# Performance work log

Measured on AMD Instinct MI355X. Metric: run time of the kernel, lower is better.

The kernel has to match this reference:

```python
import jax, jax.numpy as jnp
import numpy as np

TEMPERATURE = 0.5
BATCH_SIZE = 4096
EPS = 1e-8  # torch.nn.CosineSimilarity default eps


def setup_inputs() -> dict:
    key = jax.random.key(0)
    k1, k2 = jax.random.split(key)
    z1 = jax.random.normal(k1, (BATCH_SIZE, 256), dtype=jnp.float32)
    z2 = jax.random.normal(k2, (BATCH_SIZE, 256), dtype=jnp.float32)
    return {"z1": z1, "z2": z2}


def reference(z1, z2):
    B = z1.shape[0]
    N = 2 * B
    reps = jnp.concatenate([z1, z2], axis=0)  # [N, D]
    # Cosine similarity (torch clamps each norm to eps before dividing)
    norms = jnp.maximum(jnp.linalg.norm(reps, axis=1, keepdims=True), EPS)
    z = reps / norms
    sim = z @ z.T  # [N, N] cosine similarity matrix

    # positives: diagonals at offsets +B and -B (they are identical by symmetry,
    # but keep the original concat order: [diag(+B), diag(-B)])
    l_pos = jnp.diagonal(sim, offset=B)
    r_pos = jnp.diagonal(sim, offset=-B)
    positives = jnp.concatenate([l_pos, r_pos])  # [N]

    inv_t = 1.0 / TEMPERATURE
    pos_logit = positives * inv_t  # logits[:, 0]

    # negatives are all off-diagonal entries of each row (the positive pair is
    # thus present twice in the logits, faithful to the original). CE with
    # label 0 => loss_i = logsumexp(logits_i) - logits_i[0].
    neg_logits = jnp.where(jnp.eye(N, dtype=bool), -jnp.inf, sim * inv_t)
    lse = jnp.logaddexp(pos_logit, jax.scipy.special.logsumexp(neg_logits, axis=1))
    loss = jnp.sum(lse - pos_logit) / N
    return loss
```

## Files before the change

### kernel.cpp

```cpp
#include <hip/hip_runtime.h>
#include <hip/hip_bf16.h>
#include <cstdint>
#include <cstddef>
#include <math.h>

#define BSZ   4096
#define NROW  8192
#define DIM   256
#define INV_T 2.0f
#define EPS_N 1e-8f

typedef __attribute__((ext_vector_type(4))) float f32x4;

__device__ __forceinline__ void load_lds16(const void* g, void* l) {
    __builtin_amdgcn_global_load_lds(
        (const __attribute__((address_space(1))) void*)g,
        (__attribute__((address_space(3))) void*)l,
        16, 0, 0);
}

__global__ __launch_bounds__(256)
void nt_normalize(const float* __restrict__ z1,
                  const float* __restrict__ z2,
                  char* __restrict__ zn3,
                  float* __restrict__ rowsum) {
    const int wave = threadIdx.x >> 6;
    const int lane = threadIdx.x & 63;
    const int row  = blockIdx.x * 4 + wave;
    const float* src = (row < BSZ) ? (z1 + (size_t)row * DIM)
                                   : (z2 + (size_t)(row - BSZ) * DIM);
    const float4 v = ((const float4*)src)[lane];
    float ss = v.x * v.x + v.y * v.y + v.z * v.z + v.w * v.w;
    #pragma unroll
    for (int off = 32; off; off >>= 1) ss += __shfl_xor(ss, off);
    const float rinv = 1.0f / fmaxf(sqrtf(ss), EPS_N);
    int pk = 0;
    pk = __builtin_amdgcn_cvt_pk_fp8_f32(v.x * rinv, v.y * rinv, pk, false);
    pk = __builtin_amdgcn_cvt_pk_fp8_f32(v.z * rinv, v.w * rinv, pk, true);
    const int s    = row >> 7;
    const int lrow = row & 127;
    const int kc   = lane >> 4;
    const int unit = (lane >> 1) & 7;
    const int off4 = (lane & 1) * 4;
    const int u    = unit ^ (lrow & 7);
    *(int*)(zn3 + (size_t)s * 32768 + kc * 8192 + lrow * 64 + u * 8 + off4) = pk;
    if (lane == 0) rowsum[row] = 0.0f;
}

__global__ __launch_bounds__(256)
void nt_gram(const char* __restrict__ zn3,
             float* __restrict__ rowsum,
             float* __restrict__ pos) {
    const int l = blockIdx.x;
    int bi = (int)((129.0 - sqrt(16641.0 - 8.0 * (double)l)) * 0.5);
    while (64 * (bi + 1) - (bi + 1) * bi / 2 <= l) ++bi;
    while (64 * bi - bi * (bi - 1) / 2 > l) --bi;
    const int bj = bi + (l - (64 * bi - bi * (bi - 1) / 2));

    __shared__ char As[8192];
    __shared__ char Bs[8192];

    const int t    = threadIdx.x;
    const int lane = t & 63;
    const int wave = t >> 6;
    const int wrow = (wave >> 1) * 64;
    const int wcol = (wave & 1) * 64;
    const int q    = lane >> 4;
    const int r16  = lane & 15;
    const int sw   = r16 & 7;
    const int t16  = t * 16;

    const char* A2 = zn3 + (size_t)bi * 32768;
    const char* B2 = zn3 + (size_t)bj * 32768;

    f32x4 acc[4][4] = {};

    for (int kc = 0; kc < 4; ++kc) {
        load_lds16(A2 + kc * 8192 + t16,        As + t16);
        load_lds16(A2 + kc * 8192 + 4096 + t16, As + 4096 + t16);
        load_lds16(B2 + kc * 8192 + t16,        Bs + t16);
        load_lds16(B2 + kc * 8192 + 4096 + t16, Bs + 4096 + t16);
        __syncthreads();

        #pragma unroll
        for (int kh = 0; kh < 2; ++kh) {
            const int spos = (((kh << 2) + q) ^ sw) << 3;
            long af[4], bfv[4];
            #pragma unroll
            for (int mi = 0; mi < 4; ++mi)
                af[mi] = *(const long*)(As + (wrow + mi * 16 + r16) * 64 + spos);
            #pragma unroll
            for (int ni = 0; ni < 4; ++ni)
                bfv[ni] = *(const long*)(Bs + (wcol + ni * 16 + r16) * 64 + spos);
            #pragma unroll
            for (int mi = 0; mi < 4; ++mi)
                #pragma unroll
                for (int ni = 0; ni < 4; ++ni)
                    acc[mi][ni] = __builtin_amdgcn_mfma_f32_16x16x32_fp8_fp8(
                        af[mi], bfv[ni], acc[mi][ni], 0, 0, 0);
        }
        __syncthreads();
    }

    const int c = r16;
    const bool diag_block = (bi == bj);
    float colp[4] = {0.f, 0.f, 0.f, 0.f};

    #pragma unroll
    for (int mi = 0; mi < 4; ++mi) {
        #pragma unroll
        for (int r = 0; r < 4; ++r) {
            const int grow = bi * 128 + wrow + mi * 16 + q * 4 + r;
            float s = 0.f;
            #pragma unroll
            for (int ni = 0; ni < 4; ++ni) {
                const int gcol = bj * 128 + wcol + ni * 16 + c;
                const float val = acc[mi][ni][r];
                float e = __expf(val * INV_T);
                e = (grow == gcol) ? 0.f : e;
                s += e;
                colp[ni] += e;
                if (gcol == grow + BSZ) {
                    pos[grow] = val;
                    pos[gcol] = val;
                }
            }
            s += __shfl_xor(s, 1);
            s += __shfl_xor(s, 2);
            s += __shfl_xor(s, 4);
            s += __shfl_xor(s, 8);
            if (c == 0) atomicAdd(&rowsum[grow], s);
        }
    }
    if (!diag_block) {
        #pragma unroll
        for (int ni = 0; ni < 4; ++ni) {
            float cs = colp[ni];
            cs += __shfl_xor(cs, 16);
            cs += __shfl_xor(cs, 32);
            if (q == 0) atomicAdd(&rowsum[bj * 128 + wcol + ni * 16 + c], cs);
        }
    }
}

__global__ __launch_bounds__(1024)
void nt_finalize(const float* __restrict__ rowsum,
                 const float* __restrict__ pos,
                 float* __restrict__ out) {
    const float4* rs4 = (const float4*)rowsum;
    const float4* ps4 = (const float4*)pos;
    float v = 0.f;
    #pragma unroll
    for (int it = 0; it < 2; ++it) {
        const int i = it * 1024 + threadIdx.x;
        const float4 r = rs4[i];
        const float4 p = ps4[i];
        v += logf(__expf(p.x * INV_T) + r.x) - p.x * INV_T;
        v += logf(__expf(p.y * INV_T) + r.y) - p.y * INV_T;
        v += logf(__expf(p.z * INV_T) + r.z) - p.z * INV_T;
        v += logf(__expf(p.w * INV_T) + r.w) - p.w * INV_T;
    }
    #pragma unroll
    for (int off = 32; off; off >>= 1) v += __shfl_xor(v, off);
    __shared__ float redf[16];
    if ((threadIdx.x & 63) == 0) redf[threadIdx.x >> 6] = v;
    __syncthreads();
    if (threadIdx.x == 0) {
        float s = 0.f;
        #pragma unroll
        for (int w = 0; w < 16; ++w) s += redf[w];
        out[0] = s * (1.0f / NROW);
    }
}

extern "C" void kernel_launch(void* const* d_in, const int* in_sizes, int n_in,
                              void* d_out, int out_size, void* d_ws, size_t ws_size,
                              hipStream_t stream) {
    const float* z1 = (const float*)d_in[0];
    const float* z2 = (const float*)d_in[1];
    float* out = (float*)d_out;

    char*  zn3    = (char*)d_ws;
    float* rowsum = (float*)((char*)d_ws + (size_t)NROW * DIM);
    float* pos    = rowsum + NROW;

    nt_normalize<<<NROW / 4, 256, 0, stream>>>(z1, z2, zn3, rowsum);
    nt_gram<<<2080, 256, 0, stream>>>(zn3, rowsum, pos);
    nt_finalize<<<1, 1024, 0, stream>>>(rowsum, pos, out);
}
```

Baseline: 100.8 us.

## Replace rowsum atomics with per-slot partial buffer and parallel finalize

After: 94.79 us. 1.06x faster.

```diff
diff --git a/kernel.cpp b/kernel.cpp
--- a/kernel.cpp
+++ b/kernel.cpp
@@ -23,7 +23,7 @@
 void nt_normalize(const float* __restrict__ z1,
                   const float* __restrict__ z2,
                   char* __restrict__ zn3,
-                  float* __restrict__ rowsum) {
+                  unsigned int* __restrict__ cnt) {
     const int wave = threadIdx.x >> 6;
     const int lane = threadIdx.x & 63;
     const int row  = blockIdx.x * 4 + wave;
@@ -44,12 +44,12 @@
     const int off4 = (lane & 1) * 4;
     const int u    = unit ^ (lrow & 7);
     *(int*)(zn3 + (size_t)s * 32768 + kc * 8192 + lrow * 64 + u * 8 + off4) = pk;
-    if (lane == 0) rowsum[row] = 0.0f;
+    if (row == 0 && lane == 0) *cnt = 0;
 }
 
 __global__ __launch_bounds__(256)
 void nt_gram(const char* __restrict__ zn3,
-             float* __restrict__ rowsum,
+             float* __restrict__ part,
              float* __restrict__ pos) {
     const int l = blockIdx.x;
     int bi = (int)((129.0 - sqrt(16641.0 - 8.0 * (double)l)) * 0.5);
@@ -104,6 +104,8 @@
 
     const int c = r16;
     const bool diag_block = (bi == bj);
+    const int rslot = 2 * bj + (wcol >> 6);
+    const int cslot = 2 * bi + (wrow >> 6);
     float colp[4] = {0.f, 0.f, 0.f, 0.f};
 
     #pragma unroll
@@ -129,7 +131,7 @@
             s += __shfl_xor(s, 2);
             s += __shfl_xor(s, 4);
             s += __shfl_xor(s, 8);
-            if (c == 0) atomicAdd(&rowsum[grow], s);
+            if (c == 0) part[(size_t)grow * 128 + rslot] = s;
         }
     }
     if (!diag_block) {
@@ -138,38 +140,54 @@
             float cs = colp[ni];
             cs += __shfl_xor(cs, 16);
             cs += __shfl_xor(cs, 32);
-            if (q == 0) atomicAdd(&rowsum[bj * 128 + wcol + ni * 16 + c], cs);
+            if (q == 0)
+                part[(size_t)(bj * 128 + wcol + ni * 16 + c) * 128 + cslot] = cs;
         }
     }
 }
 
-__global__ __launch_bounds__(1024)
-void nt_finalize(const float* __restrict__ rowsum,
+__global__ __launch_bounds__(256)
+void nt_finalize(const float* __restrict__ part,
                  const float* __restrict__ pos,
+                 float* __restrict__ blocksum,
+                 unsigned int* __restrict__ cnt,
                  float* __restrict__ out) {
-    const float4* rs4 = (const float4*)rowsum;
-    const float4* ps4 = (const float4*)pos;
-    float v = 0.f;
-    #pragma unroll
-    for (int it = 0; it < 2; ++it) {
-        const int i = it * 1024 + threadIdx.x;
-        const float4 r = rs4[i];
-        const float4 p = ps4[i];
-        v += logf(__expf(p.x * INV_T) + r.x) - p.x * INV_T;
-        v += logf(__expf(p.y * INV_T) + r.y) - p.y * INV_T;
-        v += logf(__expf(p.z * INV_T) + r.z) - p.z * INV_T;
-        v += logf(__expf(p.w * INV_T) + r.w) - p.w * INV_T;
-    }
-    #pragma unroll
-    for (int off = 32; off; off >>= 1) v += __shfl_xor(v, off);
-    __shared__ float redf[16];
-    if ((threadIdx.x & 63) == 0) redf[threadIdx.x >> 6] = v;
+    const int b    = blockIdx.x;
+    const int t    = threadIdx.x;
+    const int lane = t & 63;
+    const int row  = b * 128 + (t >> 1);
+    const int half = t & 1;
+
+    const float4* p4 = (const float4*)(part + (size_t)row * 128 + half * 64);
+    float s = 0.f;
+    #pragma unroll
+    for (int j = 0; j < 16; ++j) {
+        const float4 v = p4[j];
+        s += v.x + v.y + v.z + v.w;
+    }
+    s += __shfl_xor(s, 1);
+    float contrib = 0.f;
+    if (half == 0) {
+        const float pl = pos[row] * INV_T;
+        contrib = logf(__expf(pl) + s) - pl;
+    }
+    #pragma unroll
+    for (int off = 32; off; off >>= 1) contrib += __shfl_xor(contrib, off);
+    __shared__ float r4[4];
+    __shared__ int   slast;
+    if (lane == 0) r4[t >> 6] = contrib;
     __syncthreads();
-    if (threadIdx.x == 0) {
-        float s = 0.f;
-        #pragma unroll
-        for (int w = 0; w < 16; ++w) s += redf[w];
-        out[0] = s * (1.0f / NROW);
+    if (t == 0) {
+        blocksum[b] = r4[0] + r4[1] + r4[2] + r4[3];
+        __threadfence();
+        slast = (atomicAdd(cnt, 1u) == 63u);
+    }
+    __syncthreads();
+    if (slast && t < 64) {
+        float v = atomicAdd(&blocksum[t], 0.0f);
+        #pragma unroll
+        for (int off = 32; off; off >>= 1) v += __shfl_xor(v, off);
+        if (t == 0) out[0] = v * (1.0f / NROW);
     }
 }
 
@@ -180,11 +198,13 @@
     const float* z2 = (const float*)d_in[1];
     float* out = (float*)d_out;
 
-    char*  zn3    = (char*)d_ws;
-    float* rowsum = (float*)((char*)d_ws + (size_t)NROW * DIM);
-    float* pos    = rowsum + NROW;
-
-    nt_normalize<<<NROW / 4, 256, 0, stream>>>(z1, z2, zn3, rowsum);
-    nt_gram<<<2080, 256, 0, stream>>>(zn3, rowsum, pos);
-    nt_finalize<<<1, 1024, 0, stream>>>(rowsum, pos, out);
-}
+    char*  zn3      = (char*)d_ws;
+    float* part     = (float*)((char*)d_ws + (size_t)2097152);
+    float* pos      = (float*)((char*)d_ws + (size_t)6291456);
+    float* blocksum = pos + NROW;
+    unsigned int* cnt = (unsigned int*)(blocksum + 64);
+
+    nt_normalize<<<NROW / 4, 256, 0, stream>>>(z1, z2, zn3, cnt);
+    nt_gram<<<2080, 256, 0, stream>>>(zn3, part, pos);
+    nt_finalize<<<64, 256, 0, stream>>>(part, pos, blocksum, cnt, out);
+}
```
